# Kernel optimization log

Hardware: AMD Instinct MI355X
Metric: run time of the kernel (lower is better)

## Reference

```python
import jax, jax.numpy as jnp
import numpy as np

B, S, D = 1, 65536, 1024
NH = 8
HD = D // NH
M = 8          # memory_tokens
HID = 2048     # d_model * mlp_ratio(2.0)
EPS_LN = 1e-5
EPS_L = 1e-9


def setup_inputs() -> dict:
    key = jax.random.key(0)
    ks = jax.random.split(key, 16)
    def w(k, shape, s=0.02):
        return jax.random.normal(k, shape, dtype=jnp.float32) * s
    return {
        "h_img_seq": jax.random.normal(ks[0], (B, S, D), dtype=jnp.float32),
        "latents": w(ks[1], (M, D)),
        "wq": w(ks[2], (D, D)), "bq": jnp.zeros((D,), jnp.float32),
        "wk": w(ks[3], (D, D)), "bk": jnp.zeros((D,), jnp.float32),
        "wv": w(ks[4], (D, D)), "bv": jnp.zeros((D,), jnp.float32),
        "wo": w(ks[5], (D, D)), "bo": jnp.zeros((D,), jnp.float32),
        "ln_g": jnp.ones((D,), jnp.float32), "ln_b": jnp.zeros((D,), jnp.float32),
        "w1": w(ks[6], (D, HID)), "b1": jnp.zeros((HID,), jnp.float32),
        "w2": w(ks[7], (HID, D)), "b2": jnp.zeros((D,), jnp.float32),
    }


def reference(h_img_seq, latents, wq, bq, wk, bk, wv, bv, wo, bo,
              ln_g, ln_b, w1, b1, w2, b2):
    b, s, d = h_img_seq.shape
    scale = HD ** -0.5
    # queries from latents: [M, NH, HD] (shared across batch)
    q = (latents @ wq + bq).reshape(M, NH, HD).astype(jnp.float32)
    # K/V projections over the long sequence: [B, S, NH, HD] (fp32 accum)
    k = (h_img_seq @ wk + bk).reshape(b, s, NH, HD).astype(jnp.float32)
    v = (h_img_seq @ wv + bv).reshape(b, s, NH, HD).astype(jnp.float32)
    # online-softmax over chunks == stable softmax over full S (denominator l + 1e-9)
    logits = jnp.einsum('mhd,bshd->bhms', q, k) * scale          # [B, NH, M, S]
    mmax = jnp.max(logits, axis=-1, keepdims=True)
    e = jnp.exp(logits - mmax)
    l = jnp.sum(e, axis=-1, keepdims=True)                       # [B, NH, M, 1]
    acc = jnp.einsum('bhms,bshd->bhmd', e, v)                    # [B, NH, M, HD]
    out = acc / (l + EPS_L)
    out = out.transpose(0, 2, 1, 3).reshape(b, M, d).astype(h_img_seq.dtype)
    out = out @ wo + bo
    # MLP: LayerNorm -> Linear -> GELU(exact) -> Linear, residual
    mu = jnp.mean(out, axis=-1, keepdims=True)
    var = jnp.mean((out - mu) ** 2, axis=-1, keepdims=True)
    h = (out - mu) * jax.lax.rsqrt(var + EPS_LN) * ln_g + ln_b
    h = jax.nn.gelu(h @ w1 + b1, approximate=False) @ w2 + b2
    out = out + h
    m_vec = out.mean(axis=1)
    return (out, m_vec)
```

## Files before the change

### kernel.cpp

```cpp
#include <hip/hip_runtime.h>
#include <stdint.h>
#include <math.h>

#define S_LEN   65536
#define DM      1024
#define HD_     128
#define HID_    2048
#define SCALE_F 0.08838834764831845f

typedef float          f32x4  __attribute__((ext_vector_type(4)));
typedef short          bf16x8 __attribute__((ext_vector_type(8)));
typedef unsigned short u16;

__device__ __forceinline__ u16 f2bf(float f) {
  union { float f; uint32_t u; } v; v.f = f;
  uint32_t u = v.u;
  u += 0x7FFFu + ((u >> 16) & 1u);
  return (u16)(u >> 16);
}

__device__ __forceinline__ bf16x8 pack_bf8(const float* f) {
  union { bf16x8 v; u16 s[8]; } r;
#pragma unroll
  for (int i = 0; i < 8; ++i) r.s[i] = f2bf(f[i]);
  return r.v;
}

#define WS_Q      0u
#define WS_QKA    32768u
#define WS_QBK    163840u
#define WS_GMAX   164096u
#define WS_LSUM   164352u
#define WS_PLSUM  164608u
#define WS_XN     167936u
#define WS_EWH    430080u
#define WS_PMAX   430080u
#define WS_OATT   692224u
#define WS_O2     724992u
#define WS_H1     757760u
#define WS_PBASE  1048576u
#define WS_LOGITS 1048576u
#define WS_PEW    1048576u
#define WS_E      34603008u

template<int KS>
__global__ __launch_bounds__(256) void k_sk8(const float* __restrict__ X,
                                             const float* __restrict__ W,
                                             float* __restrict__ P,
                                             int C, int K, int ncg) {
  int cg = blockIdx.x % ncg, kb = blockIdx.x / ncg;
  int c = (cg << 9) + threadIdx.x * 2;
  int k0 = kb * KS;
  float2 acc[8];
#pragma unroll
  for (int r = 0; r < 8; ++r) { acc[r].x = 0.f; acc[r].y = 0.f; }
  const float* wp = W + (size_t)k0 * C + c;
#pragma unroll 8
  for (int i = 0; i < KS; ++i) {
    float2 w = *(const float2*)wp; wp += C;
#pragma unroll
    for (int r = 0; r < 8; ++r) {
      float xv = X[r * K + k0 + i];
      acc[r].x += xv * w.x; acc[r].y += xv * w.y;
    }
  }
  float* pp = P + (size_t)(kb * 8) * C + c;
#pragma unroll
  for (int r = 0; r < 8; ++r) *(float2*)(pp + (size_t)r * C) = acc[r];
}

__global__ __launch_bounds__(256) void k_sk8h(const float* __restrict__ ewh,
                                              const float* __restrict__ wv,
                                              float* __restrict__ Pa) {
  int h = blockIdx.x & 7, kb = blockIdx.x >> 3;
  int lane = threadIdx.x & 63, q4 = threadIdx.x >> 6;
  int c = h * 128 + lane * 2;
  int k0 = kb * 64 + q4 * 16;
  const float* xp = ewh + h * 8192 + k0 * 8;
  const float* wp = wv + (size_t)k0 * 1024 + c;
  float2 acc[8];
#pragma unroll
  for (int m = 0; m < 8; ++m) { acc[m].x = 0.f; acc[m].y = 0.f; }
#pragma unroll
  for (int i = 0; i < 16; ++i) {
    float2 w = *(const float2*)wp; wp += 1024;
#pragma unroll
    for (int m = 0; m < 8; ++m) {
      float xv = xp[i * 8 + m];
      acc[m].x += xv * w.x; acc[m].y += xv * w.y;
    }
  }
  int slab = kb * 4 + q4;
  float* pp = Pa + (size_t)(slab * 8) * 1024 + c;
#pragma unroll
  for (int m = 0; m < 8; ++m) *(float2*)(pp + (size_t)m * 1024) = acc[m];
}

__global__ void k_red_q(const float* __restrict__ P, const float* __restrict__ bq,
                        float* __restrict__ q) {
  int idx = blockIdx.x * 256 + threadIdx.x;
  int m = idx >> 10, c = idx & 1023;
  float s = bq[c];
#pragma unroll 8
  for (int ks = 0; ks < 32; ++ks) s += P[(size_t)(ks * 8 + m) * 1024 + c];
  q[idx] = s;
}

__global__ void k_qbk(const float* __restrict__ q, const float* __restrict__ bk,
                      float* __restrict__ qbk) {
  int t = threadIdx.x;
  int r = t >> 2, qr = t & 3;
  int m = r >> 3, h = r & 7;
  float s = 0.f;
  int d0 = qr * 32;
#pragma unroll
  for (int d = 0; d < 32; ++d)
    s += q[m * 1024 + h * 128 + d0 + d] * bk[h * 128 + d0 + d];
  s += __shfl_xor(s, 1);
  s += __shfl_xor(s, 2);
  if (qr == 0) qbk[r] = s * SCALE_F;
}

__global__ __launch_bounds__(256) void k_foldqk(const float* __restrict__ q,
                                                const float* __restrict__ wk,
                                                u16* __restrict__ qka) {
  __shared__ float tile[64 * 129];
  int h = blockIdx.x & 7, ib = blockIdx.x >> 3;
  int i0 = ib * 64;
  int t = threadIdx.x;
  {
    int ii = t >> 2, dg = (t & 3) * 32;
    const float* src = wk + (size_t)(i0 + ii) * 1024 + h * 128 + dg;
    float* dst = tile + ii * 129 + dg;
#pragma unroll
    for (int u = 0; u < 8; ++u) {
      f32x4 v = *(const f32x4*)(src + u * 4);
      dst[u * 4 + 0] = v[0]; dst[u * 4 + 1] = v[1];
      dst[u * 4 + 2] = v[2]; dst[u * 4 + 3] = v[3];
    }
  }
  __syncthreads();
  int ii = t & 63, q4 = t >> 6;
  int i = i0 + ii;
  float a0 = 0.f, a1 = 0.f;
#pragma unroll 16
  for (int d = 0; d < 128; ++d) {
    float w = tile[ii * 129 + d];
    a0 += q[(q4 * 2 + 0) * 1024 + h * 128 + d] * w;
    a1 += q[(q4 * 2 + 1) * 1024 + h * 128 + d] * w;
  }
#pragma unroll
  for (int j = 0; j < 2; ++j) {
    int m = q4 * 2 + j;
    int r = m * 8 + h;
    float val = (j == 0 ? a0 : a1) * SCALE_F;
    int K0 = i >> 5, rb = r >> 4, hi = (i & 31) >> 3, e = i & 7, l16 = r & 15;
    int lane = hi * 16 + l16;
    qka[(((K0 * 4 + rb) * 64 + lane) << 3) + e] = f2bf(val);
  }
}

__global__ __launch_bounds__(256, 4) void k_logits(
    const float* __restrict__ h, const u16* __restrict__ qka,
    const float* __restrict__ qbk, float* __restrict__ logits,
    float* __restrict__ pmax) {
  __shared__ __align__(16) u16 Abuf[2][2048];
  __shared__ float pmL[4 * 64];
  int t = threadIdx.x, wg = blockIdx.x;
  int w = t >> 6, l = t & 63;
  int g = l >> 4, l15 = l & 15;
  int scol = wg * 64 + w * 16 + l15;

  ((uint4*)Abuf[0])[t] = ((const uint4*)qka)[t];
  __syncthreads();

  f32x4 acc[4];
#pragma unroll
  for (int rb = 0; rb < 4; ++rb) acc[rb] = (f32x4){0.f, 0.f, 0.f, 0.f};

  for (int ks = 0; ks < 32; ++ks) {
    int buf = ks & 1;
    if (ks + 1 < 32)
      ((uint4*)Abuf[buf ^ 1])[t] = ((const uint4*)(qka + (size_t)(ks + 1) * 2048))[t];
    const float* hp = h + (size_t)scol * DM + ks * 32 + g * 8;
    float fb[8];
    f32x4 f0 = *(const f32x4*)hp;
    f32x4 f1 = *(const f32x4*)(hp + 4);
    fb[0]=f0[0]; fb[1]=f0[1]; fb[2]=f0[2]; fb[3]=f0[3];
    fb[4]=f1[0]; fb[5]=f1[1]; fb[6]=f1[2]; fb[7]=f1[3];
    bf16x8 bfr = pack_bf8(fb);
    const bf16x8* ap = (const bf16x8*)Abuf[buf];
#pragma unroll
    for (int rb = 0; rb < 4; ++rb) {
      bf16x8 af = ap[rb * 64 + l];
      acc[rb] = __builtin_amdgcn_mfma_f32_16x16x32_bf16(af, bfr, acc[rb], 0, 0, 0);
    }
    __syncthreads();
  }

#pragma unroll
  for (int rb = 0; rb < 4; ++rb) {
#pragma unroll
    for (int j = 0; j < 4; ++j) {
      int r = rb * 16 + g * 4 + j;
      float val = acc[rb][j] + qbk[r];
      logits[(size_t)r * S_LEN + scol] = val;
      float mx = val;
      mx = fmaxf(mx, __shfl_xor(mx, 1));
      mx = fmaxf(mx, __shfl_xor(mx, 2));
      mx = fmaxf(mx, __shfl_xor(mx, 4));
      mx = fmaxf(mx, __shfl_xor(mx, 8));
      if (l15 == 0) pmL[w * 64 + r] = mx;
    }
  }
  __syncthreads();
  if (t < 64) {
    float m0 = fmaxf(fmaxf(pmL[t], pmL[64 + t]), fmaxf(pmL[128 + t], pmL[192 + t]));
    pmax[(size_t)t * 1024 + wg] = m0;
  }
}

__global__ void k_gmax(const float* __restrict__ pmax, float* __restrict__ gmax) {
  int r = blockIdx.x, t = threadIdx.x;
  __shared__ float red[256];
  float m = -3.0e38f;
  for (int i = t; i < 1024; i += 256) m = fmaxf(m, pmax[(size_t)r * 1024 + i]);
  red[t] = m; __syncthreads();
  for (int s = 128; s > 0; s >>= 1) {
    if (t < s) red[t] = fmaxf(red[t], red[t + s]);
    __syncthreads();
  }
  if (t == 0) gmax[r] = red[0];
}

__global__ void k_make_e(const float* __restrict__ logits, const float* __restrict__ gmax,
                         u16* __restrict__ E, float* __restrict__ plsum) {
  int b = blockIdx.x, t = threadIdx.x;
  int r = b >> 3, sc = b & 7;
  float gm = gmax[r];
  size_t base = (size_t)r * S_LEN + sc * 8192 + t * 32;
  const float* lp = logits + base;
  u16* ep = E + base;
  float sum = 0.f;
#pragma unroll
  for (int gi = 0; gi < 4; ++gi) {
    f32x4 f0 = *(const f32x4*)(lp + gi * 8);
    f32x4 f1 = *(const f32x4*)(lp + gi * 8 + 4);
    float e[8];
#pragma unroll
    for (int i = 0; i < 4; ++i) { e[i] = expf(f0[i] - gm); e[4 + i] = expf(f1[i] - gm); }
    union { uint4 u4; u16 s[8]; } pk;
#pragma unroll
    for (int i = 0; i < 8; ++i) { sum += e[i]; pk.s[i] = f2bf(e[i]); }
    *(uint4*)(ep + gi * 8) = pk.u4;
  }
  __shared__ float red[256];
  red[t] = sum; __syncthreads();
  for (int s = 128; s > 0; s >>= 1) {
    if (t < s) red[t] += red[t + s];
    __syncthreads();
  }
  if (t == 0) plsum[r * 8 + sc] = red[0];
}

__global__ __launch_bounds__(256, 4) void k_pass2(
    const float* __restrict__ h, const u16* __restrict__ E, float* __restrict__ pew) {
  int t = threadIdx.x;
  int chunk = blockIdx.x >> 3, ctile = blockIdx.x & 7;
  int w = t >> 6, l = t & 63;
  int g = l >> 4, l15 = l & 15;
  int c0 = ctile * 128 + w * 32;
  f32x4 acc[4][2];
#pragma unroll
  for (int rb = 0; rb < 4; ++rb)
#pragma unroll
    for (int cb = 0; cb < 2; ++cb) acc[rb][cb] = (f32x4){0.f, 0.f, 0.f, 0.f};

  int kbase = chunk * 512;
  for (int ks = 0; ks < 16; ++ks) {
    int k0 = kbase + ks * 32;
    bf16x8 af[4];
#pragma unroll
    for (int rb = 0; rb < 4; ++rb) {
      size_t eidx = (size_t)(rb * 16 + l15) * S_LEN + k0 + g * 8;
      uint4 u = *(const uint4*)(E + eidx);
      af[rb] = *(bf16x8*)&u;
    }
    bf16x8 bfb[2];
#pragma unroll
    for (int cb = 0; cb < 2; ++cb) {
      const float* hp = h + (size_t)(k0 + g * 8) * DM + c0 + cb * 16 + l15;
      float fb[8];
#pragma unroll
      for (int e = 0; e < 8; ++e) fb[e] = hp[(size_t)e * DM];
      bfb[cb] = pack_bf8(fb);
    }
#pragma unroll
    for (int rb = 0; rb < 4; ++rb)
#pragma unroll
      for (int cb = 0; cb < 2; ++cb)
        acc[rb][cb] = __builtin_amdgcn_mfma_f32_16x16x32_bf16(af[rb], bfb[cb], acc[rb][cb], 0, 0, 0);
  }
  float* pw = pew + (size_t)chunk * 65536;
#pragma unroll
  for (int rb = 0; rb < 4; ++rb)
#pragma unroll
    for (int cb = 0; cb < 2; ++cb)
#pragma unroll
      for (int j = 0; j < 4; ++j) {
        int r = rb * 16 + g * 4 + j;
        int c = c0 + cb * 16 + l15;
        pw[(size_t)r * 1024 + c] = acc[rb][cb][j];
      }
}

__global__ void k_red_ew(const float* __restrict__ pew, float* __restrict__ ewh,
                         const float* __restrict__ plsum, float* __restrict__ lsum) {
  int idx = blockIdx.x * 256 + threadIdx.x;
  const float* p = pew + idx;
  float s = 0.f;
#pragma unroll 8
  for (int ch = 0; ch < 128; ++ch) s += p[(size_t)ch * 65536];
  int r = idx >> 10, c = idx & 1023;
  int m = r >> 3, hh = r & 7;
  ewh[hh * 8192 + c * 8 + m] = s;
  if (blockIdx.x == 0 && threadIdx.x < 64) {
    float lv = 0.f;
#pragma unroll
    for (int i = 0; i < 8; ++i) lv += plsum[threadIdx.x * 8 + i];
    lsum[threadIdx.x] = lv;
  }
}

__global__ void k_red_attn(const float* __restrict__ Pa, const float* __restrict__ lsum,
                           const float* __restrict__ bv, float* __restrict__ oatt) {
  int idx = blockIdx.x * 256 + threadIdx.x;
  int m = idx >> 10, col = idx & 1023;
  int r = m * 8 + (col >> 7);
  float s = 0.f;
#pragma unroll 8
  for (int ks = 0; ks < 64; ++ks) s += Pa[(size_t)(ks * 8 + m) * 1024 + col];
  float lv = lsum[r];
  oatt[idx] = (s + lv * bv[col]) / (lv + 1e-9f);
}

__global__ void k_red_o2(const float* __restrict__ P, const float* __restrict__ bo,
                         float* __restrict__ o2) {
  int idx = blockIdx.x * 256 + threadIdx.x;
  int m = idx >> 10, c = idx & 1023;
  float s = bo[c];
#pragma unroll 8
  for (int ks = 0; ks < 32; ++ks) s += P[(size_t)(ks * 8 + m) * 1024 + c];
  o2[idx] = s;
}

__global__ void k_ln(const float* __restrict__ o2, const float* __restrict__ g,
                     const float* __restrict__ b, float* __restrict__ xn) {
  int m = blockIdx.x, t = threadIdx.x;
  __shared__ float red[256], red2[256];
  f32x4 x = ((const f32x4*)(o2 + m * 1024))[t];
  float s = x[0] + x[1] + x[2] + x[3];
  float s2 = x[0]*x[0] + x[1]*x[1] + x[2]*x[2] + x[3]*x[3];
  red[t] = s; red2[t] = s2; __syncthreads();
  for (int st = 128; st > 0; st >>= 1) {
    if (t < st) { red[t] += red[t + st]; red2[t] += red2[t + st]; }
    __syncthreads();
  }
  float mu = red[0] * (1.f / DM);
  float var = fmaxf(red2[0] * (1.f / DM) - mu * mu, 0.f);
  float rstd = rsqrtf(var + 1e-5f);
  f32x4 gg = ((const f32x4*)g)[t];
  f32x4 bb = ((const f32x4*)b)[t];
  f32x4 o;
#pragma unroll
  for (int j = 0; j < 4; ++j) o[j] = (x[j] - mu) * rstd * gg[j] + bb[j];
  ((f32x4*)(xn + m * 1024))[t] = o;
}

__global__ void k_red_h1(const float* __restrict__ P, const float* __restrict__ b1,
                         float* __restrict__ h1) {
  int idx = blockIdx.x * 256 + threadIdx.x;
  int m = idx >> 11, j = idx & 2047;
  float s = b1[j];
#pragma unroll 8
  for (int ks = 0; ks < 32; ++ks) s += P[(size_t)(ks * 8 + m) * 2048 + j];
  h1[idx] = 0.5f * s * (1.f + erff(s * 0.70710678118654752f));
}

__global__ void k_red_out(const float* __restrict__ P, const float* __restrict__ b2,
                          const float* __restrict__ o2, float* __restrict__ out) {
  int idx = blockIdx.x * 256 + threadIdx.x;
  int m = idx >> 10, c = idx & 1023;
  float s = b2[c];
#pragma unroll 8
  for (int ks = 0; ks < 64; ++ks) s += P[(size_t)(ks * 8 + m) * 1024 + c];
  out[idx] = o2[idx] + s;
}

__global__ void k_mvec(float* __restrict__ out) {
  int j = blockIdx.x * 256 + threadIdx.x;
  float s = 0.f;
#pragma unroll
  for (int m = 0; m < 8; ++m) s += out[m * DM + j];
  out[8192 + j] = s * 0.125f;
}

extern "C" void kernel_launch(void* const* d_in, const int* in_sizes, int n_in,
                              void* d_out, int out_size, void* d_ws, size_t ws_size,
                              hipStream_t stream) {
  (void)in_sizes; (void)n_in; (void)out_size; (void)ws_size;
  const float* h   = (const float*)d_in[0];
  const float* lat = (const float*)d_in[1];
  const float* wq  = (const float*)d_in[2];
  const float* bq  = (const float*)d_in[3];
  const float* wk  = (const float*)d_in[4];
  const float* bk  = (const float*)d_in[5];
  const float* wv  = (const float*)d_in[6];
  const float* bv  = (const float*)d_in[7];
  const float* wo  = (const float*)d_in[8];
  const float* bo  = (const float*)d_in[9];
  const float* lng = (const float*)d_in[10];
  const float* lnb = (const float*)d_in[11];
  const float* w1  = (const float*)d_in[12];
  const float* b1  = (const float*)d_in[13];
  const float* w2  = (const float*)d_in[14];
  const float* b2  = (const float*)d_in[15];
  float* out = (float*)d_out;
  char* ws = (char*)d_ws;

  float* q      = (float*)(ws + WS_Q);
  u16*   qka    = (u16*)  (ws + WS_QKA);
  float* qbk    = (float*)(ws + WS_QBK);
  float* gmax   = (float*)(ws + WS_GMAX);
  float* lsum   = (float*)(ws + WS_LSUM);
  float* plsum  = (float*)(ws + WS_PLSUM);
  float* xn     = (float*)(ws + WS_XN);
  float* ewh    = (float*)(ws + WS_EWH);
  float* pmax   = (float*)(ws + WS_PMAX);
  float* oatt   = (float*)(ws + WS_OATT);
  float* o2     = (float*)(ws + WS_O2);
  float* h1     = (float*)(ws + WS_H1);
  float* P      = (float*)(ws + WS_PBASE);
  float* logits = (float*)(ws + WS_LOGITS);
  float* pew    = (float*)(ws + WS_PEW);
  u16*   E      = (u16*)  (ws + WS_E);

  hipLaunchKernelGGL((k_sk8<32>), dim3(64),  dim3(256), 0, stream, lat, wq, P, 1024, 1024, 2);
  hipLaunchKernelGGL(k_red_q,     dim3(32),  dim3(256), 0, stream, P, bq, q);
  hipLaunchKernelGGL(k_qbk,       dim3(1),   dim3(256), 0, stream, q, bk, qbk);
  hipLaunchKernelGGL(k_foldqk,    dim3(128), dim3(256), 0, stream, q, wk, qka);
  hipLaunchKernelGGL(k_logits,    dim3(1024), dim3(256), 0, stream, h, qka, qbk, logits, pmax);
  hipLaunchKernelGGL(k_gmax,      dim3(64),  dim3(256), 0, stream, pmax, gmax);
  hipLaunchKernelGGL(k_make_e,    dim3(512), dim3(256), 0, stream, logits, gmax, E, plsum);
  hipLaunchKernelGGL(k_pass2,     dim3(1024), dim3(256), 0, stream, h, E, pew);
  hipLaunchKernelGGL(k_red_ew,    dim3(256), dim3(256), 0, stream, pew, ewh, plsum, lsum);
  hipLaunchKernelGGL(k_sk8h,      dim3(128), dim3(256), 0, stream, ewh, wv, P);
  hipLaunchKernelGGL(k_red_attn,  dim3(32),  dim3(256), 0, stream, P, lsum, bv, oatt);
  hipLaunchKernelGGL((k_sk8<32>), dim3(64),  dim3(256), 0, stream, oatt, wo, P, 1024, 1024, 2);
  hipLaunchKernelGGL(k_red_o2,    dim3(32),  dim3(256), 0, stream, P, bo, o2);
  hipLaunchKernelGGL(k_ln,        dim3(8),   dim3(256), 0, stream, o2, lng, lnb, xn);
  hipLaunchKernelGGL((k_sk8<32>), dim3(128), dim3(256), 0, stream, xn, w1, P, 2048, 1024, 4);
  hipLaunchKernelGGL(k_red_h1,    dim3(64),  dim3(256), 0, stream, P, b1, h1);
  hipLaunchKernelGGL((k_sk8<32>), dim3(128), dim3(256), 0, stream, h1, w2, P, 1024, 2048, 2);
  hipLaunchKernelGGL(k_red_out,   dim3(32),  dim3(256), 0, stream, P, b2, o2, out);
  hipLaunchKernelGGL(k_mvec,      dim3(4),   dim3(256), 0, stream, out);
}
```

Baseline: 583.8 us.

## Fuse small kernels, drop LDS staging in logits, halve pass2 chunks

Folds qbk into foldqk, gmax into make_e, red_o2 into layernorm, and mvec into the final reduction, cutting launches from 19 to 15. The logits kernel now reads qka fragments straight from global/L2 instead of double-buffering them through LDS with per-step barriers, and occupancy hints are relaxed. pass2 handles 1024-row chunks with half as many blocks, so the partial-sum reduction reads half as many slabs. The trade-off is that every wave re-reads qka from cache, and pass2 runs fewer, longer blocks, which may underfill the GPU.

```diff
diff --git a/kernel.cpp b/kernel.cpp
--- a/kernel.cpp
+++ b/kernel.cpp
@@ -29,18 +29,17 @@
 #define WS_Q      0u
 #define WS_QKA    32768u
 #define WS_QBK    163840u
-#define WS_GMAX   164096u
 #define WS_LSUM   164352u
 #define WS_PLSUM  164608u
 #define WS_XN     167936u
 #define WS_EWH    430080u
-#define WS_PMAX   430080u
-#define WS_OATT   692224u
-#define WS_O2     724992u
-#define WS_H1     757760u
-#define WS_PBASE  1048576u
-#define WS_LOGITS 1048576u
-#define WS_PEW    1048576u
+#define WS_PMAX   698368u
+#define WS_OATT   960512u
+#define WS_O2     993280u
+#define WS_H1     1026048u
+#define WS_PBASE  2097152u
+#define WS_LOGITS 2097152u
+#define WS_PEW    2097152u
 #define WS_E      34603008u
 
 template<int KS>
@@ -106,28 +105,26 @@
   q[idx] = s;
 }
 
-__global__ void k_qbk(const float* __restrict__ q, const float* __restrict__ bk,
-                      float* __restrict__ qbk) {
-  int t = threadIdx.x;
-  int r = t >> 2, qr = t & 3;
-  int m = r >> 3, h = r & 7;
-  float s = 0.f;
-  int d0 = qr * 32;
-#pragma unroll
-  for (int d = 0; d < 32; ++d)
-    s += q[m * 1024 + h * 128 + d0 + d] * bk[h * 128 + d0 + d];
-  s += __shfl_xor(s, 1);
-  s += __shfl_xor(s, 2);
-  if (qr == 0) qbk[r] = s * SCALE_F;
-}
-
 __global__ __launch_bounds__(256) void k_foldqk(const float* __restrict__ q,
                                                 const float* __restrict__ wk,
-                                                u16* __restrict__ qka) {
+                                                const float* __restrict__ bk,
+                                                u16* __restrict__ qka,
+                                                float* __restrict__ qbk) {
   __shared__ float tile[64 * 129];
   int h = blockIdx.x & 7, ib = blockIdx.x >> 3;
   int i0 = ib * 64;
   int t = threadIdx.x;
+  if (ib == 0 && t < 64) {
+    int m = t >> 3, part = t & 7;
+    float s = 0.f;
+#pragma unroll
+    for (int d = 0; d < 16; ++d)
+      s += q[m * 1024 + h * 128 + part * 16 + d] * bk[h * 128 + part * 16 + d];
+    s += __shfl_xor(s, 1);
+    s += __shfl_xor(s, 2);
+    s += __shfl_xor(s, 4);
+    if (part == 0) qbk[m * 8 + h] = s * SCALE_F;
+  }
   {
     int ii = t >> 2, dg = (t & 3) * 32;
     const float* src = wk + (size_t)(i0 + ii) * 1024 + h * 128 + dg;
@@ -160,28 +157,23 @@
   }
 }
 
-__global__ __launch_bounds__(256, 4) void k_logits(
+__global__ __launch_bounds__(256) void k_logits(
     const float* __restrict__ h, const u16* __restrict__ qka,
     const float* __restrict__ qbk, float* __restrict__ logits,
     float* __restrict__ pmax) {
-  __shared__ __align__(16) u16 Abuf[2][2048];
   __shared__ float pmL[4 * 64];
   int t = threadIdx.x, wg = blockIdx.x;
   int w = t >> 6, l = t & 63;
   int g = l >> 4, l15 = l & 15;
   int scol = wg * 64 + w * 16 + l15;
-
-  ((uint4*)Abuf[0])[t] = ((const uint4*)qka)[t];
-  __syncthreads();
+  const bf16x8* qf = (const bf16x8*)qka;
 
   f32x4 acc[4];
 #pragma unroll
   for (int rb = 0; rb < 4; ++rb) acc[rb] = (f32x4){0.f, 0.f, 0.f, 0.f};
 
+#pragma unroll 2
   for (int ks = 0; ks < 32; ++ks) {
-    int buf = ks & 1;
-    if (ks + 1 < 32)
-      ((uint4*)Abuf[buf ^ 1])[t] = ((const uint4*)(qka + (size_t)(ks + 1) * 2048))[t];
     const float* hp = h + (size_t)scol * DM + ks * 32 + g * 8;
     float fb[8];
     f32x4 f0 = *(const f32x4*)hp;
@@ -189,13 +181,11 @@
     fb[0]=f0[0]; fb[1]=f0[1]; fb[2]=f0[2]; fb[3]=f0[3];
     fb[4]=f1[0]; fb[5]=f1[1]; fb[6]=f1[2]; fb[7]=f1[3];
     bf16x8 bfr = pack_bf8(fb);
-    const bf16x8* ap = (const bf16x8*)Abuf[buf];
 #pragma unroll
     for (int rb = 0; rb < 4; ++rb) {
-      bf16x8 af = ap[rb * 64 + l];
+      bf16x8 af = qf[(ks * 4 + rb) * 64 + l];
       acc[rb] = __builtin_amdgcn_mfma_f32_16x16x32_bf16(af, bfr, acc[rb], 0, 0, 0);
     }
-    __syncthreads();
   }
 
 #pragma unroll
@@ -220,24 +210,22 @@
   }
 }
 
-__global__ void k_gmax(const float* __restrict__ pmax, float* __restrict__ gmax) {
-  int r = blockIdx.x, t = threadIdx.x;
+__global__ void k_make_e(const float* __restrict__ logits, const float* __restrict__ pmax,
+                         u16* __restrict__ E, float* __restrict__ plsum) {
+  int b = blockIdx.x, t = threadIdx.x;
+  int r = b >> 3, sc = b & 7;
   __shared__ float red[256];
-  float m = -3.0e38f;
-  for (int i = t; i < 1024; i += 256) m = fmaxf(m, pmax[(size_t)r * 1024 + i]);
-  red[t] = m; __syncthreads();
+  float mv = -3.0e38f;
+#pragma unroll
+  for (int i = 0; i < 4; ++i) mv = fmaxf(mv, pmax[(size_t)r * 1024 + t + i * 256]);
+  red[t] = mv; __syncthreads();
   for (int s = 128; s > 0; s >>= 1) {
     if (t < s) red[t] = fmaxf(red[t], red[t + s]);
     __syncthreads();
   }
-  if (t == 0) gmax[r] = red[0];
-}
-
-__global__ void k_make_e(const float* __restrict__ logits, const float* __restrict__ gmax,
-                         u16* __restrict__ E, float* __restrict__ plsum) {
-  int b = blockIdx.x, t = threadIdx.x;
-  int r = b >> 3, sc = b & 7;
-  float gm = gmax[r];
+  float gm = red[0];
+  __syncthreads();
+
   size_t base = (size_t)r * S_LEN + sc * 8192 + t * 32;
   const float* lp = logits + base;
   u16* ep = E + base;
@@ -254,7 +242,6 @@
     for (int i = 0; i < 8; ++i) { sum += e[i]; pk.s[i] = f2bf(e[i]); }
     *(uint4*)(ep + gi * 8) = pk.u4;
   }
-  __shared__ float red[256];
   red[t] = sum; __syncthreads();
   for (int s = 128; s > 0; s >>= 1) {
     if (t < s) red[t] += red[t + s];
@@ -263,7 +250,7 @@
   if (t == 0) plsum[r * 8 + sc] = red[0];
 }
 
-__global__ __launch_bounds__(256, 4) void k_pass2(
+__global__ __launch_bounds__(256) void k_pass2(
     const float* __restrict__ h, const u16* __restrict__ E, float* __restrict__ pew) {
   int t = threadIdx.x;
   int chunk = blockIdx.x >> 3, ctile = blockIdx.x & 7;
@@ -276,8 +263,9 @@
 #pragma unroll
     for (int cb = 0; cb < 2; ++cb) acc[rb][cb] = (f32x4){0.f, 0.f, 0.f, 0.f};
 
-  int kbase = chunk * 512;
-  for (int ks = 0; ks < 16; ++ks) {
+  int kbase = chunk * 1024;
+#pragma unroll 2
+  for (int ks = 0; ks < 32; ++ks) {
     int k0 = kbase + ks * 32;
     bf16x8 af[4];
 #pragma unroll
@@ -320,7 +308,7 @@
   const float* p = pew + idx;
   float s = 0.f;
 #pragma unroll 8
-  for (int ch = 0; ch < 128; ++ch) s += p[(size_t)ch * 65536];
+  for (int ch = 0; ch < 64; ++ch) s += p[(size_t)ch * 65536];
   int r = idx >> 10, c = idx & 1023;
   int m = r >> 3, hh = r & 7;
   ewh[hh * 8192 + c * 8 + m] = s;
@@ -344,23 +332,21 @@
   oatt[idx] = (s + lv * bv[col]) / (lv + 1e-9f);
 }
 
-__global__ void k_red_o2(const float* __restrict__ P, const float* __restrict__ bo,
-                         float* __restrict__ o2) {
-  int idx = blockIdx.x * 256 + threadIdx.x;
-  int m = idx >> 10, c = idx & 1023;
-  float s = bo[c];
-#pragma unroll 8
-  for (int ks = 0; ks < 32; ++ks) s += P[(size_t)(ks * 8 + m) * 1024 + c];
-  o2[idx] = s;
-}
-
-__global__ void k_ln(const float* __restrict__ o2, const float* __restrict__ g,
-                     const float* __restrict__ b, float* __restrict__ xn) {
+__global__ void k_red_o2_ln(const float* __restrict__ P, const float* __restrict__ bo,
+                            const float* __restrict__ g, const float* __restrict__ b,
+                            float* __restrict__ o2, float* __restrict__ xn) {
   int m = blockIdx.x, t = threadIdx.x;
   __shared__ float red[256], red2[256];
-  f32x4 x = ((const f32x4*)(o2 + m * 1024))[t];
-  float s = x[0] + x[1] + x[2] + x[3];
-  float s2 = x[0]*x[0] + x[1]*x[1] + x[2]*x[2] + x[3]*x[3];
+  f32x4 s4 = ((const f32x4*)bo)[t];
+#pragma unroll 8
+  for (int ks = 0; ks < 32; ++ks) {
+    f32x4 p = ((const f32x4*)(P + (size_t)(ks * 8 + m) * 1024))[t];
+#pragma unroll
+    for (int j = 0; j < 4; ++j) s4[j] += p[j];
+  }
+  ((f32x4*)(o2 + m * 1024))[t] = s4;
+  float s = s4[0] + s4[1] + s4[2] + s4[3];
+  float s2 = s4[0]*s4[0] + s4[1]*s4[1] + s4[2]*s4[2] + s4[3]*s4[3];
   red[t] = s; red2[t] = s2; __syncthreads();
   for (int st = 128; st > 0; st >>= 1) {
     if (t < st) { red[t] += red[t + st]; red2[t] += red2[t + st]; }
@@ -373,7 +359,7 @@
   f32x4 bb = ((const f32x4*)b)[t];
   f32x4 o;
 #pragma unroll
-  for (int j = 0; j < 4; ++j) o[j] = (x[j] - mu) * rstd * gg[j] + bb[j];
+  for (int j = 0; j < 4; ++j) o[j] = (s4[j] - mu) * rstd * gg[j] + bb[j];
   ((f32x4*)(xn + m * 1024))[t] = o;
 }
 
@@ -387,22 +373,20 @@
   h1[idx] = 0.5f * s * (1.f + erff(s * 0.70710678118654752f));
 }
 
-__global__ void k_red_out(const float* __restrict__ P, const float* __restrict__ b2,
-                          const float* __restrict__ o2, float* __restrict__ out) {
+__global__ void k_red_out_mvec(const float* __restrict__ P, const float* __restrict__ b2,
+                               const float* __restrict__ o2, float* __restrict__ out) {
   int idx = blockIdx.x * 256 + threadIdx.x;
-  int m = idx >> 10, c = idx & 1023;
-  float s = b2[c];
-#pragma unroll 8
-  for (int ks = 0; ks < 64; ++ks) s += P[(size_t)(ks * 8 + m) * 1024 + c];
-  out[idx] = o2[idx] + s;
-}
-
-__global__ void k_mvec(float* __restrict__ out) {
-  int j = blockIdx.x * 256 + threadIdx.x;
-  float s = 0.f;
-#pragma unroll
-  for (int m = 0; m < 8; ++m) s += out[m * DM + j];
-  out[8192 + j] = s * 0.125f;
+  int j = idx >> 3, m = idx & 7;
+  float s = b2[j];
+#pragma unroll 8
+  for (int ks = 0; ks < 64; ++ks) s += P[(size_t)(ks * 8 + m) * 1024 + j];
+  s += o2[m * 1024 + j];
+  out[m * 1024 + j] = s;
+  float sm = s;
+  sm += __shfl_xor(sm, 1);
+  sm += __shfl_xor(sm, 2);
+  sm += __shfl_xor(sm, 4);
+  if (m == 0) out[8192 + j] = sm * 0.125f;
 }
 
 extern "C" void kernel_launch(void* const* d_in, const int* in_sizes, int n_in,
@@ -431,7 +415,6 @@
   float* q      = (float*)(ws + WS_Q);
   u16*   qka    = (u16*)  (ws + WS_QKA);
   float* qbk    = (float*)(ws + WS_QBK);
-  float* gmax   = (float*)(ws + WS_GMAX);
   float* lsum   = (float*)(ws + WS_LSUM);
   float* plsum  = (float*)(ws + WS_PLSUM);
   float* xn     = (float*)(ws + WS_XN);
@@ -447,21 +430,17 @@
 
   hipLaunchKernelGGL((k_sk8<32>), dim3(64),  dim3(256), 0, stream, lat, wq, P, 1024, 1024, 2);
   hipLaunchKernelGGL(k_red_q,     dim3(32),  dim3(256), 0, stream, P, bq, q);
-  hipLaunchKernelGGL(k_qbk,       dim3(1),   dim3(256), 0, stream, q, bk, qbk);
-  hipLaunchKernelGGL(k_foldqk,    dim3(128), dim3(256), 0, stream, q, wk, qka);
+  hipLaunchKernelGGL(k_foldqk,    dim3(128), dim3(256), 0, stream, q, wk, bk, qka, qbk);
   hipLaunchKernelGGL(k_logits,    dim3(1024), dim3(256), 0, stream, h, qka, qbk, logits, pmax);
-  hipLaunchKernelGGL(k_gmax,      dim3(64),  dim3(256), 0, stream, pmax, gmax);
-  hipLaunchKernelGGL(k_make_e,    dim3(512), dim3(256), 0, stream, logits, gmax, E, plsum);
-  hipLaunchKernelGGL(k_pass2,     dim3(1024), dim3(256), 0, stream, h, E, pew);
+  hipLaunchKernelGGL(k_make_e,    dim3(512), dim3(256), 0, stream, logits, pmax, E, plsum);
+  hipLaunchKernelGGL(k_pass2,     dim3(512), dim3(256), 0, stream, h, E, pew);
   hipLaunchKernelGGL(k_red_ew,    dim3(256), dim3(256), 0, stream, pew, ewh, plsum, lsum);
   hipLaunchKernelGGL(k_sk8h,      dim3(128), dim3(256), 0, stream, ewh, wv, P);
   hipLaunchKernelGGL(k_red_attn,  dim3(32),  dim3(256), 0, stream, P, lsum, bv, oatt);
   hipLaunchKernelGGL((k_sk8<32>), dim3(64),  dim3(256), 0, stream, oatt, wo, P, 1024, 1024, 2);
-  hipLaunchKernelGGL(k_red_o2,    dim3(32),  dim3(256), 0, stream, P, bo, o2);
-  hipLaunchKernelGGL(k_ln,        dim3(8),   dim3(256), 0, stream, o2, lng, lnb, xn);
+  hipLaunchKernelGGL(k_red_o2_ln, dim3(8),   dim3(256), 0, stream, P, bo, lng, lnb, o2, xn);
   hipLaunchKernelGGL((k_sk8<32>), dim3(128), dim3(256), 0, stream, xn, w1, P, 2048, 1024, 4);
   hipLaunchKernelGGL(k_red_h1,    dim3(64),  dim3(256), 0, stream, P, b1, h1);
   hipLaunchKernelGGL((k_sk8<32>), dim3(128), dim3(256), 0, stream, h1, w2, P, 1024, 2048, 2);
-  hipLaunchKernelGGL(k_red_out,   dim3(32),  dim3(256), 0, stream, P, b2, o2, out);
-  hipLaunchKernelGGL(k_mvec,      dim3(4),   dim3(256), 0, stream, out);
-}
+  hipLaunchKernelGGL(k_red_out_mvec, dim3(32), dim3(256), 0, stream, P, b2, o2, out);
+}
```

Result: faster. 563.4 us (-3.5%).
